# Kernel tuning notes

Measured on AMD Instinct MI355X. Metric: run time of the kernel, lower is better.

## Reference

```python
import jax, jax.numpy as jnp
import numpy as np

N, E, CIN, H, OUT, L, G = 100000, 1600000, 64, 128, 16, 3, 64

def setup_inputs() -> dict:
    key = jax.random.key(0)
    ks = jax.random.split(key, 20)
    def xav(k, shape):
        fan_in, fan_out = shape[-2], shape[-1]
        lim = float(np.sqrt(6.0 / (fan_in + fan_out)))
        return jax.random.uniform(k, shape, jnp.float32, -lim, lim)
    inp = {
        "x": jax.random.normal(ks[0], (N, CIN), jnp.float32),
        "pos": jax.random.normal(ks[1], (N, 3), jnp.float32),
        "edge_index": jax.random.randint(ks[2], (2, E), 0, N, jnp.int64),
        "batch": jnp.sort(jax.random.randint(ks[3], (N,), 0, G, jnp.int64)),
        # node_lin: Linear(CIN+3, H) -> ReLU -> Linear(H, H)
        "node_w1": xav(ks[4], (CIN + 3, H)), "node_b1": jnp.zeros((H,), jnp.float32),
        "node_w2": xav(ks[5], (H, H)), "node_b2": jnp.zeros((H,), jnp.float32),
        # L convs, each with [L, H, H] propagation weights and a GRUCell
        "conv_w": xav(ks[6], (L, L, H, H)),
        "gru_wih": xav(ks[7], (L, 3 * H, H)), "gru_whh": xav(ks[8], (L, 3 * H, H)),
        "gru_bih": jnp.zeros((L, 3 * H), jnp.float32), "gru_bhh": jnp.zeros((L, 3 * H), jnp.float32),
        "lin1_w": xav(ks[9], (H, H // 2)), "lin1_b": jnp.zeros((H // 2,), jnp.float32),
        "lin2_w": xav(ks[10], (H // 2, OUT)), "lin2_b": jnp.zeros((OUT,), jnp.float32),
    }
    return inp

def _gru_cell(m, h, wih, whh, bih, bhh):
    # torch.nn.GRUCell semantics: gates = [r, z, n]
    gi = m @ wih.T + bih  # [N, 3H]
    gh = h @ whh.T + bhh
    ir, iz, inn = jnp.split(gi, 3, axis=1)
    hr, hz, hn = jnp.split(gh, 3, axis=1)
    r = jax.nn.sigmoid(ir + hr)
    z = jax.nn.sigmoid(iz + hz)
    n = jnp.tanh(inn + r * hn)
    return (1.0 - z) * n + z * h

def reference(x, pos, edge_index, batch, node_w1, node_b1, node_w2, node_b2,
              conv_w, gru_wih, gru_whh, gru_bih, gru_bhh,
              lin1_w, lin1_b, lin2_w, lin2_b):
    src, dst = edge_index[0], edge_index[1]  # message flows src -> dst
    h = jnp.concatenate([x, pos], axis=1)
    h = jax.nn.relu(h @ node_w1 + node_b1) @ node_w2 + node_b2
    for l in range(L):  # GatedNet outer convs
        for i in range(L):  # GatedGraphConv inner iterations
            m = h @ conv_w[l, i]                                  # [N, H]
            agg = jax.ops.segment_sum(m[src], dst, num_segments=N)  # gather + scatter-add
            h = _gru_cell(agg, h, gru_wih[l], gru_whh[l], gru_bih[l], gru_bhh[l])
        h = jax.nn.relu(h)
    h = jax.nn.relu(h @ lin1_w + lin1_b)
    h = h @ lin2_w + lin2_b                                        # [N, OUT]
    return jax.ops.segment_sum(h, batch, num_segments=G)           # graph readout 'add'
```

## Files before the change

kernel.cpp:

```cpp
#include <hip/hip_runtime.h>

#define NN 100000
#define NE 1600000
#define NG 64
#define MAXDEG 64

typedef long long i64;
typedef unsigned short u16;
typedef __attribute__((ext_vector_type(8))) _Float16 f16x8;
typedef __attribute__((ext_vector_type(4))) _Float16 half4;
typedef __attribute__((ext_vector_type(4))) float f32x4;

__device__ __forceinline__ float sigm(float x){ return 1.f/(1.f+__expf(-x)); }
__device__ __forceinline__ float tanh_(float x){ return 2.f/(1.f+__expf(-2.f*x)) - 1.f; }
__device__ __forceinline__ f32x4 mfma16h(f16x8 a, f16x8 b, f32x4 c){
  return __builtin_amdgcn_mfma_f32_16x16x32_f16(a,b,c,0,0,0);
}

__global__ __launch_bounds__(512) void k_detect(const int* __restrict__ ei,
    const int* __restrict__ batch, int* __restrict__ flags){
  int t = threadIdx.x;
  __shared__ int nz_e, nz_b;
  if (t == 0){ nz_e = 0; nz_b = 0; }
  __syncthreads();
  if (ei[2*t + 1] != 0) nz_e = 1;
  int k = NN/2 - 512 + t;
  if (batch[2*k + 1] != 0) nz_b = 1;
  __syncthreads();
  if (t == 0){ flags[0] = nz_e ? 0 : 1; flags[1] = nz_b ? 0 : 1; }
}

__global__ __launch_bounds__(256) void k_prep_wT(const float* __restrict__ wih,
    const float* __restrict__ whh, float* __restrict__ wihT, float* __restrict__ whhT){
  int idx = blockIdx.x*256 + threadIdx.x;
  if (idx >= 3*49152) return;
  int l = idx/49152, r = idx - l*49152, k = r/384, jc = r - k*384;
  wihT[idx] = wih[((size_t)l*384 + jc)*128 + k];
  whhT[idx] = whh[((size_t)l*384 + jc)*128 + k];
}

__global__ __launch_bounds__(384) void k_weff(const float* __restrict__ convw,
    const float* __restrict__ wihT, float* __restrict__ WeffT){
  int bid = blockIdx.x;
  int li = bid >> 7, k = bid & 127;
  int l = li / 3;
  int j = threadIdx.x;
  __shared__ float cwrow[128];
  if (j < 128) cwrow[j] = convw[((size_t)li*128 + k)*128 + j];
  __syncthreads();
  const float* wT = wihT + (size_t)l*49152;
  float acc = 0.f;
#pragma unroll 8
  for (int m = 0; m < 128; ++m)
    acc = fmaf(cwrow[m], wT[(size_t)m*384 + j], acc);
  WeffT[(size_t)li*49152 + (size_t)k*384 + j] = acc;
}

__global__ __launch_bounds__(256) void k_bsplit(const float* __restrict__ WeffT,
    const float* __restrict__ whhT, u16* __restrict__ Bhi, u16* __restrict__ Blo){
  int idx = blockIdx.x*256 + threadIdx.x;
  int li = idx >> 17;
  int r = idx & 131071;
  int col = r >> 8, k = r & 255;
  int l = li / 3;
  float v = 0.f;
  if (k < 128){
    if (col < 384) v = WeffT[(size_t)li*49152 + (size_t)k*384 + col];
  } else {
    int k2 = k - 128;
    if (col < 256)       v = whhT[(size_t)l*49152 + (size_t)k2*384 + col];
    else if (col >= 384) v = whhT[(size_t)l*49152 + (size_t)k2*384 + (col-128)];
  }
  _Float16 hi = (_Float16)v;
  _Float16 lo = (_Float16)(v - (float)hi);
  size_t widx = (size_t)li*131072 + ((((size_t)(k>>5))*512 + col)*4 + ((k>>3)&3))*8 + (k&7);
  Bhi[widx] = *(const u16*)&hi;
  Blo[widx] = *(const u16*)&lo;
}

__global__ __launch_bounds__(256) void k_fill_edges(const int* __restrict__ ei,
    const int* __restrict__ flags, int* __restrict__ deg, int* __restrict__ col){
  int e = blockIdx.x*256 + threadIdx.x;
  if (e >= NE) return;
  int s, d;
  if (flags[0]){
    const i64* e64 = (const i64*)ei;
    s = (int)e64[e]; d = (int)e64[NE + e];
  } else {
    s = ei[e]; d = ei[NE + e];
  }
  int slot = atomicAdd(&deg[d], 1);
  if (slot < MAXDEG) col[(size_t)d*MAXDEG + slot] = s;
}

__global__ __launch_bounds__(128) void k_enc_n(const float* __restrict__ x,
    const float* __restrict__ pos, const float* __restrict__ w1, const float* __restrict__ b1,
    const float* __restrict__ w2, const float* __restrict__ b2, float* __restrict__ h){
  int n0 = blockIdx.x * 8, j = threadIdx.x;
  __shared__ float xr[8][68];
  __shared__ float t1[8][128];
  for (int q = j; q < 8*67; q += 128){
    int p = q/67, kk = q - p*67;
    xr[p][kk] = (kk < 64) ? x[(size_t)(n0+p)*64 + kk] : pos[(size_t)(n0+p)*3 + (kk-64)];
  }
  __syncthreads();
  float s[8];
#pragma unroll
  for (int p=0;p<8;++p) s[p] = b1[j];
  for (int k=0;k<67;++k){
    float w = w1[k*128 + j];
#pragma unroll
    for (int p=0;p<8;++p) s[p] = fmaf(xr[p][k], w, s[p]);
  }
#pragma unroll
  for (int p=0;p<8;++p) t1[p][j] = fmaxf(s[p], 0.f);
  __syncthreads();
#pragma unroll
  for (int p=0;p<8;++p) s[p] = b2[j];
  for (int k=0;k<128;++k){
    float w = w2[k*128 + j];
#pragma unroll
    for (int p=0;p<8;++p) s[p] = fmaf(t1[p][k], w, s[p]);
  }
#pragma unroll
  for (int p=0;p<8;++p) h[(size_t)(n0+p)*128 + j] = s[p];
}

__global__ __launch_bounds__(256) void k_spmm(const int* __restrict__ deg,
    const int* __restrict__ col, const float* __restrict__ h, float* __restrict__ ah){
  int node = (blockIdx.x<<2) + (threadIdx.x>>6);
  int lane = threadIdx.x & 63;
  int d = deg[node]; d = min(d, MAXDEG);
  int mysrc = col[(size_t)node*MAXDEG + lane];
  float ax = 0.f, ay = 0.f;
  for (int s = 0; s < d; ++s){
    int src = __shfl(mysrc, s, 64);
    float2 v = *(const float2*)(h + (size_t)src*128 + (lane<<1));
    ax += v.x; ay += v.y;
  }
  float2 o; o.x = ax; o.y = ay;
  *(float2*)(ah + (size_t)node*128 + (lane<<1)) = o;
}

__global__ __launch_bounds__(512, 4) void k_gru_mfma(const float* __restrict__ ah,
    float* __restrict__ h, const u16* __restrict__ Bhi, const u16* __restrict__ Blo,
    const float* __restrict__ bih, const float* __restrict__ bhh, int apply_relu){
  __shared__ u16 Ahi[64*256];
  __shared__ u16 Alo[64*256];
  const int tid = threadIdx.x, lane = tid & 63, w = tid >> 6;
  const int tile = blockIdx.x * 64;

#pragma unroll
  for (int half = 0; half < 2; ++half){
    const float* src = half ? h : ah;
#pragma unroll
    for (int i = 0; i < 4; ++i){
      int f = i*512 + tid;
      int row = f >> 5, colq = f & 31;
      int n = tile + row;
      float4 v = {0.f,0.f,0.f,0.f};
      if (n < NN) v = *(const float4*)(src + (size_t)n*128 + colq*4);
      int colu = half*128 + colq*4;
      int chunk = colu >> 3, e4 = colu & 7;
      int cs = chunk ^ (row & 7);
      int idx = row*256 + cs*8 + e4;
      _Float16 h0=(_Float16)v.x, h1=(_Float16)v.y, h2=(_Float16)v.z, h3=(_Float16)v.w;
      _Float16 l0=(_Float16)(v.x-(float)h0), l1=(_Float16)(v.y-(float)h1),
               l2=(_Float16)(v.z-(float)h2), l3=(_Float16)(v.w-(float)h3);
      half4 hv = {h0,h1,h2,h3};
      half4 lv = {l0,l1,l2,l3};
      *(half4*)(Ahi + idx) = hv;
      *(half4*)(Alo + idx) = lv;
    }
  }
  __syncthreads();

  const f32x4 fz = {0.f,0.f,0.f,0.f};
  f32x4 acc[4][4];
#pragma unroll
  for (int g=0;g<4;++g)
#pragma unroll
    for (int R=0;R<4;++R) acc[g][R] = fz;

#pragma unroll
  for (int kk = 0; kk < 8; ++kk){
    f16x8 a_hi[4], a_lo[4];
#pragma unroll
    for (int R=0;R<4;++R){
      int arow = R*16 + (lane&15);
      int cs = (kk*4 + (lane>>4)) ^ (arow & 7);
      a_hi[R] = *(const f16x8*)(Ahi + arow*256 + cs*8);
      a_lo[R] = *(const f16x8*)(Alo + arow*256 + cs*8);
    }
#pragma unroll
    for (int g=0; g<4; ++g){
      if (g==2 && kk>=4) continue;
      if (g==3 && kk<4) continue;
      int colg = g*128 + w*16 + (lane&15);
      size_t boff = (((size_t)kk*512 + colg)*4 + (lane>>4))*8;
      f16x8 bh = *(const f16x8*)(Bhi + boff);
      f16x8 bl = *(const f16x8*)(Blo + boff);
#pragma unroll
      for (int R=0;R<4;++R){
        acc[g][R] = mfma16h(a_hi[R], bh, acc[g][R]);
        acc[g][R] = mfma16h(a_hi[R], bl, acc[g][R]);
        acc[g][R] = mfma16h(a_lo[R], bh, acc[g][R]);
      }
    }
  }

  {
    int jj = w*16 + (lane&15);
    float br  = bih[jj]     + bhh[jj];
    float bz  = bih[128+jj] + bhh[128+jj];
    float bin = bih[256+jj];
    float bhn = bhh[256+jj];
#pragma unroll
    for (int R=0;R<4;++R)
#pragma unroll
      for (int v=0;v<4;++v){
        int r_ = R*16 + ((lane>>4)<<2) + v;
        int n = tile + r_;
        float rg = sigm(acc[0][R][v] + br);
        float zg = sigm(acc[1][R][v] + bz);
        float hnv = acc[3][R][v] + bhn;
        float ng = tanh_(acc[2][R][v] + bin + rg*hnv);
        int colu = 128 + jj;
        int cs = (colu >> 3) ^ (r_ & 7);
        int lidx = r_*256 + cs*8 + (colu & 7);
        float hold = (float)(*(const _Float16*)(Ahi + lidx))
                   + (float)(*(const _Float16*)(Alo + lidx));
        float hnew = (1.f - zg)*ng + zg*hold;
        if (apply_relu) hnew = fmaxf(hnew, 0.f);
        if (n < NN) h[(size_t)n*128 + jj] = hnew;
      }
  }
}

__global__ __launch_bounds__(64) void k_head_n(const float* __restrict__ h,
    const float* __restrict__ l1, const float* __restrict__ b1,
    const float* __restrict__ l2, const float* __restrict__ b2, float* __restrict__ nodeout){
  int n0 = blockIdx.x * 8, j = threadIdx.x;
  __shared__ float hrow[8][128], t[8][64];
  for (int q = j; q < 1024; q += 64){
    int p = q >> 7, k = q & 127;
    hrow[p][k] = h[(size_t)(n0+p)*128 + k];
  }
  __syncthreads();
  float s[8];
#pragma unroll
  for (int p=0;p<8;++p) s[p] = b1[j];
  for (int k=0;k<128;++k){
    float w = l1[k*64 + j];
#pragma unroll
    for (int p=0;p<8;++p) s[p] = fmaf(hrow[p][k], w, s[p]);
  }
#pragma unroll
  for (int p=0;p<8;++p) t[p][j] = fmaxf(s[p], 0.f);
  __syncthreads();
  int c = j & 15;
#pragma unroll
  for (int pp=0;pp<2;++pp){
    int p = (j >> 4) + pp*4;
    float o = b2[c];
    for (int k=0;k<64;++k) o = fmaf(t[p][k], l2[k*16 + c], o);
    nodeout[(size_t)(n0+p)*16 + c] = o;
  }
}

__device__ __forceinline__ int lbound32(const int* __restrict__ a, int n, int v){
  int lo = 0, hi = n;
  while (lo < hi){ int mid = (lo+hi)>>1; if (a[mid] < v) lo = mid+1; else hi = mid; }
  return lo;
}
__device__ __forceinline__ int lbound64(const i64* __restrict__ a, int n, i64 v){
  int lo = 0, hi = n;
  while (lo < hi){ int mid = (lo+hi)>>1; if (a[mid] < v) lo = mid+1; else hi = mid; }
  return lo;
}
__global__ __launch_bounds__(256) void k_reduce(const float* __restrict__ nodeout,
    const int* __restrict__ batch, const int* __restrict__ flags, float* __restrict__ out){
  int g = blockIdx.x;
  int lo, hi;
  if (flags[1]){
    const i64* b64 = (const i64*)batch;
    lo = lbound64(b64, NN, (i64)g); hi = lbound64(b64, NN, (i64)g+1);
  } else {
    lo = lbound32(batch, NN, g); hi = lbound32(batch, NN, g+1);
  }
  int tid = threadIdx.x;
  int c = tid & 15, rr = tid >> 4;
  float s = 0.f;
  for (int r = lo + rr; r < hi; r += 16) s += nodeout[(size_t)r*16 + c];
  __shared__ float red[256];
  red[tid] = s; __syncthreads();
  for (int step = 128; step >= 16; step >>= 1){
    if (tid < step) red[tid] += red[tid + step];
    __syncthreads();
  }
  if (tid < 16) out[g*16 + tid] = red[tid];
}

extern "C" void kernel_launch(void* const* d_in, const int* in_sizes, int n_in,
                              void* d_out, int out_size, void* d_ws, size_t ws_size,
                              hipStream_t stream){
  const float* x        = (const float*)d_in[0];
  const float* pos      = (const float*)d_in[1];
  const int*   edge     = (const int*)d_in[2];
  const int*   batch    = (const int*)d_in[3];
  const float* node_w1  = (const float*)d_in[4];
  const float* node_b1  = (const float*)d_in[5];
  const float* node_w2  = (const float*)d_in[6];
  const float* node_b2  = (const float*)d_in[7];
  const float* conv_w   = (const float*)d_in[8];
  const float* gru_wih  = (const float*)d_in[9];
  const float* gru_whh  = (const float*)d_in[10];
  const float* gru_bih  = (const float*)d_in[11];
  const float* gru_bhh  = (const float*)d_in[12];
  const float* lin1_w   = (const float*)d_in[13];
  const float* lin1_b   = (const float*)d_in[14];
  const float* lin2_w   = (const float*)d_in[15];
  const float* lin2_b   = (const float*)d_in[16];
  float* out = (float*)d_out;

  char* p = (char*)d_ws;
  int*   flags = (int*)p;   p += 256;
  float* h     = (float*)p; p += (size_t)NN*128*4;
  float* ah    = (float*)p; p += (size_t)NN*128*4;
  float* nodeout = (float*)p; p += (size_t)NN*16*4;
  int*   deg   = (int*)p;   p += (size_t)NN*4;
  int*   col   = (int*)p;   p += (size_t)NN*MAXDEG*4;
  float* wihT  = (float*)p; p += (size_t)3*49152*4;
  float* whhT  = (float*)p; p += (size_t)3*49152*4;
  float* WeffT = (float*)p; p += (size_t)9*49152*4;
  u16*   Bhi   = (u16*)p;   p += (size_t)9*512*256*2;
  u16*   Blo   = (u16*)p;   p += (size_t)9*512*256*2;

  k_detect<<<1, 512, 0, stream>>>(edge, batch, flags);
  hipMemsetAsync(deg, 0, (size_t)NN*4, stream);
  k_prep_wT<<<(147456 + 255)/256, 256, 0, stream>>>(gru_wih, gru_whh, wihT, whhT);
  k_weff<<<9*128, 384, 0, stream>>>(conv_w, wihT, WeffT);
  k_bsplit<<<9*512*256/256, 256, 0, stream>>>(WeffT, whhT, Bhi, Blo);
  k_fill_edges<<<NE/256, 256, 0, stream>>>(edge, flags, deg, col);
  k_enc_n<<<NN/8, 128, 0, stream>>>(x, pos, node_w1, node_b1, node_w2, node_b2, h);

  for (int l = 0; l < 3; ++l){
    for (int i = 0; i < 3; ++i){
      int li = l*3 + i;
      k_spmm<<<NN/4, 256, 0, stream>>>(deg, col, h, ah);
      k_gru_mfma<<<(NN + 63)/64, 512, 0, stream>>>(ah, h, Bhi + (size_t)li*131072,
          Blo + (size_t)li*131072, gru_bih + l*384, gru_bhh + l*384, (i==2) ? 1 : 0);
    }
  }
  k_head_n<<<NN/8, 64, 0, stream>>>(h, lin1_w, lin1_b, lin2_w, lin2_b, nodeout);
  k_reduce<<<NG, 256, 0, stream>>>(nodeout, batch, flags, out);
}
```

Measured before the change: 2.150 ms.

## Fuse neighbor aggregation into GRU MFMA kernel with ping-pong h buffers

```diff
diff --git a/kernel.cpp b/kernel.cpp
--- a/kernel.cpp
+++ b/kernel.cpp
@@ -126,24 +126,9 @@
   for (int p=0;p<8;++p) h[(size_t)(n0+p)*128 + j] = s[p];
 }
 
-__global__ __launch_bounds__(256) void k_spmm(const int* __restrict__ deg,
-    const int* __restrict__ col, const float* __restrict__ h, float* __restrict__ ah){
-  int node = (blockIdx.x<<2) + (threadIdx.x>>6);
-  int lane = threadIdx.x & 63;
-  int d = deg[node]; d = min(d, MAXDEG);
-  int mysrc = col[(size_t)node*MAXDEG + lane];
-  float ax = 0.f, ay = 0.f;
-  for (int s = 0; s < d; ++s){
-    int src = __shfl(mysrc, s, 64);
-    float2 v = *(const float2*)(h + (size_t)src*128 + (lane<<1));
-    ax += v.x; ay += v.y;
-  }
-  float2 o; o.x = ax; o.y = ay;
-  *(float2*)(ah + (size_t)node*128 + (lane<<1)) = o;
-}
-
-__global__ __launch_bounds__(512, 4) void k_gru_mfma(const float* __restrict__ ah,
-    float* __restrict__ h, const u16* __restrict__ Bhi, const u16* __restrict__ Blo,
+__global__ __launch_bounds__(512, 4) void k_fused(const int* __restrict__ deg,
+    const int* __restrict__ col, const float* __restrict__ hin, float* __restrict__ hout,
+    const u16* __restrict__ Bhi, const u16* __restrict__ Blo,
     const float* __restrict__ bih, const float* __restrict__ bhh, int apply_relu){
   __shared__ u16 Ahi[64*256];
   __shared__ u16 Alo[64*256];
@@ -151,27 +136,47 @@
   const int tile = blockIdx.x * 64;
 
 #pragma unroll
-  for (int half = 0; half < 2; ++half){
-    const float* src = half ? h : ah;
-#pragma unroll
-    for (int i = 0; i < 4; ++i){
-      int f = i*512 + tid;
-      int row = f >> 5, colq = f & 31;
-      int n = tile + row;
-      float4 v = {0.f,0.f,0.f,0.f};
-      if (n < NN) v = *(const float4*)(src + (size_t)n*128 + colq*4);
-      int colu = half*128 + colq*4;
-      int chunk = colu >> 3, e4 = colu & 7;
-      int cs = chunk ^ (row & 7);
-      int idx = row*256 + cs*8 + e4;
-      _Float16 h0=(_Float16)v.x, h1=(_Float16)v.y, h2=(_Float16)v.z, h3=(_Float16)v.w;
-      _Float16 l0=(_Float16)(v.x-(float)h0), l1=(_Float16)(v.y-(float)h1),
-               l2=(_Float16)(v.z-(float)h2), l3=(_Float16)(v.w-(float)h3);
-      half4 hv = {h0,h1,h2,h3};
-      half4 lv = {l0,l1,l2,l3};
-      *(half4*)(Ahi + idx) = hv;
-      *(half4*)(Alo + idx) = lv;
+  for (int i = 0; i < 4; ++i){
+    int f = i*512 + tid;
+    int row = f >> 5, colq = f & 31;
+    int n = tile + row;
+    float4 v = {0.f,0.f,0.f,0.f};
+    if (n < NN) v = *(const float4*)(hin + (size_t)n*128 + colq*4);
+    int colu = 128 + colq*4;
+    int chunk = colu >> 3, e4 = colu & 7;
+    int cs = chunk ^ (row & 7);
+    int idx = row*256 + cs*8 + e4;
+    _Float16 h0=(_Float16)v.x, h1=(_Float16)v.y, h2=(_Float16)v.z, h3=(_Float16)v.w;
+    _Float16 l0=(_Float16)(v.x-(float)h0), l1=(_Float16)(v.y-(float)h1),
+             l2=(_Float16)(v.z-(float)h2), l3=(_Float16)(v.w-(float)h3);
+    half4 hv = {h0,h1,h2,h3};
+    half4 lv = {l0,l1,l2,l3};
+    *(half4*)(Ahi + idx) = hv;
+    *(half4*)(Alo + idx) = lv;
+  }
+
+#pragma unroll 2
+  for (int rr = 0; rr < 8; ++rr){
+    int row = w*8 + rr;
+    int node = tile + row;
+    float ax = 0.f, ay = 0.f;
+    if (node < NN){
+      int d = deg[node]; d = min(d, MAXDEG);
+      int mysrc = col[(size_t)node*MAXDEG + lane];
+      for (int s = 0; s < d; ++s){
+        int src = __shfl(mysrc, s, 64);
+        float2 v = *(const float2*)(hin + (size_t)src*128 + (lane<<1));
+        ax += v.x; ay += v.y;
+      }
     }
+    int colu = lane << 1;
+    int chunk = colu >> 3;
+    int cs = chunk ^ (row & 7);
+    int idx = row*256 + cs*8 + (colu & 7);
+    _Float16 hx=(_Float16)ax, hy=(_Float16)ay;
+    _Float16 lx=(_Float16)(ax-(float)hx), ly=(_Float16)(ay-(float)hy);
+    Ahi[idx]   = *(const u16*)&hx;  Ahi[idx+1] = *(const u16*)&hy;
+    Alo[idx]   = *(const u16*)&lx;  Alo[idx+1] = *(const u16*)&ly;
   }
   __syncthreads();
 
@@ -232,7 +237,7 @@
                    + (float)(*(const _Float16*)(Alo + lidx));
         float hnew = (1.f - zg)*ng + zg*hold;
         if (apply_relu) hnew = fmaxf(hnew, 0.f);
-        if (n < NN) h[(size_t)n*128 + jj] = hnew;
+        if (n < NN) hout[(size_t)n*128 + jj] = hnew;
       }
   }
 }
@@ -325,8 +330,8 @@
 
   char* p = (char*)d_ws;
   int*   flags = (int*)p;   p += 256;
-  float* h     = (float*)p; p += (size_t)NN*128*4;
-  float* ah    = (float*)p; p += (size_t)NN*128*4;
+  float* h0    = (float*)p; p += (size_t)NN*128*4;
+  float* h1    = (float*)p; p += (size_t)NN*128*4;
   float* nodeout = (float*)p; p += (size_t)NN*16*4;
   int*   deg   = (int*)p;   p += (size_t)NN*4;
   int*   col   = (int*)p;   p += (size_t)NN*MAXDEG*4;
@@ -342,16 +347,17 @@
   k_weff<<<9*128, 384, 0, stream>>>(conv_w, wihT, WeffT);
   k_bsplit<<<9*512*256/256, 256, 0, stream>>>(WeffT, whhT, Bhi, Blo);
   k_fill_edges<<<NE/256, 256, 0, stream>>>(edge, flags, deg, col);
-  k_enc_n<<<NN/8, 128, 0, stream>>>(x, pos, node_w1, node_b1, node_w2, node_b2, h);
-
+  k_enc_n<<<NN/8, 128, 0, stream>>>(x, pos, node_w1, node_b1, node_w2, node_b2, h0);
+
+  float* hbuf[2] = { h0, h1 };
   for (int l = 0; l < 3; ++l){
     for (int i = 0; i < 3; ++i){
       int li = l*3 + i;
-      k_spmm<<<NN/4, 256, 0, stream>>>(deg, col, h, ah);
-      k_gru_mfma<<<(NN + 63)/64, 512, 0, stream>>>(ah, h, Bhi + (size_t)li*131072,
-          Blo + (size_t)li*131072, gru_bih + l*384, gru_bhh + l*384, (i==2) ? 1 : 0);
+      k_fused<<<(NN + 63)/64, 512, 0, stream>>>(deg, col, hbuf[li & 1], hbuf[(li + 1) & 1],
+          Bhi + (size_t)li*131072, Blo + (size_t)li*131072,
+          gru_bih + l*384, gru_bhh + l*384, (i==2) ? 1 : 0);
     }
   }
-  k_head_n<<<NN/8, 64, 0, stream>>>(h, lin1_w, lin1_b, lin2_w, lin2_b, nodeout);
+  k_head_n<<<NN/8, 64, 0, stream>>>(hbuf[1], lin1_w, lin1_b, lin2_w, lin2_b, nodeout);
   k_reduce<<<NG, 256, 0, stream>>>(nodeout, batch, flags, out);
 }
```

After: 2.866 ms. +33.3%, slower.
